# Kernel optimization log

Hardware: AMD Instinct MI355X
Metric: run time of the kernel (lower is better)

Reference implementation:

```python
import jax, jax.numpy as jnp
import numpy as np

H = 16          # num_heads
R = 4           # query compression ratio
WIN = 128       # sliding window size
NEG = -1e9      # finite mask value (safe softmax grads)


def setup_inputs() -> dict:
    key = jax.random.key(0)
    k0, k1, k2, k3, k4 = jax.random.split(key, 5)
    B, S, D = 4, 4096, 2048
    inputs = jax.random.normal(k0, (B, S, D), jnp.float32)
    attention_mask = jnp.ones((B, S), jnp.int32)
    s = 0.02
    Wq = jax.random.normal(k1, (D, D), jnp.float32) * s
    Wk = jax.random.normal(k2, (D, D), jnp.float32) * s
    Wv = jax.random.normal(k3, (D, D), jnp.float32) * s
    Wo = jax.random.normal(k4, (D, D), jnp.float32) * s
    return {"inputs": inputs, "attention_mask": attention_mask,
            "Wq": Wq, "Wk": Wk, "Wv": Wv, "Wo": Wo}


def _forward(inputs, attention_mask, Wq, Wk, Wv, Wo):
    B, S, D = inputs.shape
    dh = D // H
    scale = 1.0 / np.sqrt(dh).astype(np.float32)
    Cs = (S + R - 1) // R            # compressed query length (S % R == 0 here)
    win = min(WIN, S)
    ws = max(0, S - win)             # window start

    # Q projection -> [B,H,S,dh] -> compress groups of R by mean -> [B,H,Cs,dh]
    q = jnp.einsum('bsd,od->bso', inputs, Wq)
    q = q.reshape(B, S, H, dh).transpose(0, 2, 1, 3)
    qc = q.reshape(B, H, Cs, R, dh).mean(axis=3)

    # K/V only over the recent window
    wx = inputs[:, ws:ws + win, :]
    k = jnp.einsum('bsd,od->bso', wx, Wk).reshape(B, win, H, dh).transpose(0, 2, 1, 3)
    v = jnp.einsum('bsd,od->bso', wx, Wv).reshape(B, win, H, dh).transpose(0, 2, 1, 3)

    scores = jnp.einsum('bhqd,bhkd->bhqk', qc, k) * scale

    # causal mask: each compressed query sits at position (i+1)*R-1
    qpos = (jnp.arange(Cs) + 1) * R - 1                     # [Cs]
    wpos = ws + jnp.arange(win)
    causal = wpos[None, :] <= qpos[:, None]
    qbw = qpos < ws                                         # queries fully before window
    causal = causal.at[:, 0].set(causal[:, 0] | qbw)
    pad_ok = (attention_mask[:, ws:ws + win] != 0)
    full = causal[None, None, :, :] & pad_ok[:, None, None, :]

    scores = jnp.where(full, scores, NEG)
    weights = jax.nn.softmax(scores, axis=-1)
    out = jnp.einsum('bhqk,bhkd->bhqd', weights, v)         # [B,H,Cs,dh]
    out = out.transpose(0, 2, 1, 3).reshape(B, Cs, D)
    out = jnp.einsum('bsd,od->bso', out, Wo)

    if Cs != S:  # linear interpolation back to seq_len (align_corners=False)
        out = jax.image.resize(out, (B, S, D), method='linear')
    return out


def reference(inputs, attention_mask, Wq, Wk, Wv, Wo):
    return _forward(inputs, attention_mask, Wq, Wk, Wv, Wo)
```

## Files before the change

kernel.cpp:

```cpp
#include <hip/hip_runtime.h>
#include <hip/hip_bf16.h>


typedef __attribute__((ext_vector_type(8))) short short8;
typedef __attribute__((ext_vector_type(4))) short s16x4;
typedef __attribute__((ext_vector_type(4))) float f32x4;

#define LDP 72

#define QP_STRIDE  (128 * 2048)
#define KV_STRIDE  (512 * 2048)
#define YO_STRIDE  (132 * 2048)

__device__ __forceinline__ unsigned short f2bf(float f){
  unsigned int x = __float_as_uint(f);
  return (unsigned short)((x + 0x7fffu + ((x >> 16) & 1u)) >> 16);
}
__device__ __forceinline__ unsigned int pk2(float lo, float hi){
  return ((unsigned int)f2bf(hi) << 16) | (unsigned int)f2bf(lo);
}
__device__ __forceinline__ s16x4 cvt4(float4 v){
  union { __hip_bfloat162 h[2]; s16x4 s; } r;
  float2 a; a.x = v.x; a.y = v.y;
  float2 b; b.x = v.z; b.y = v.w;
  r.h[0] = __float22bfloat162_rn(a);
  r.h[1] = __float22bfloat162_rn(b);
  return r.s;
}
__device__ __forceinline__ short8 cvt8(float4 x, float4 y){
  union { s16x4 h[2]; short8 s; } r;
  r.h[0] = cvt4(x); r.h[1] = cvt4(y);
  return r.s;
}

__global__ __launch_bounds__(256) void prep_kernel(
    const float* __restrict__ inp,
    unsigned short* __restrict__ Awx, unsigned short* __restrict__ Aq)
{
  const int idx = blockIdx.x * 256 + threadIdx.x;
  if (blockIdx.y == 0){
    const int b = idx >> 15, rem = idx & 32767;
    const int j = rem >> 8, d8 = (rem & 255) * 8;
    const float* p = inp + ((size_t)b * 4096 + 3968 + j) * 2048 + d8;
    *(short8*)&Awx[((size_t)b * 128 + j) * 2048 + d8] =
        cvt8(*(const float4*)p, *(const float4*)(p + 4));
  } else {
    if (idx >= 32768) return;
    const int b = idx >> 13, rem = idx & 8191;
    const int c = rem >> 8, d8 = (rem & 255) * 8;
    const float* p = inp + ((size_t)b * 4096 + 3968 + 4 * c) * 2048 + d8;
    float4 x0 = *(const float4*)(p);
    float4 x1 = *(const float4*)(p + 2048);
    float4 x2 = *(const float4*)(p + 4096);
    float4 x3 = *(const float4*)(p + 6144);
    float4 y0 = *(const float4*)(p + 4);
    float4 y1 = *(const float4*)(p + 2052);
    float4 y2 = *(const float4*)(p + 4100);
    float4 y3 = *(const float4*)(p + 6148);
    float4 xm, ym;
    xm.x = 0.25f * (x0.x + x1.x + x2.x + x3.x);
    xm.y = 0.25f * (x0.y + x1.y + x2.y + x3.y);
    xm.z = 0.25f * (x0.z + x1.z + x2.z + x3.z);
    xm.w = 0.25f * (x0.w + x1.w + x2.w + x3.w);
    ym.x = 0.25f * (y0.x + y1.x + y2.x + y3.x);
    ym.y = 0.25f * (y0.y + y1.y + y2.y + y3.y);
    ym.z = 0.25f * (y0.z + y1.z + y2.z + y3.z);
    ym.w = 0.25f * (y0.w + y1.w + y2.w + y3.w);
    *(short8*)&Aq[((size_t)b * 32 + c) * 2048 + d8] = cvt8(xm, ym);
  }
}

__device__ __forceinline__ void gemm_body(
    const unsigned short* __restrict__ A, const float* __restrict__ W,
    float* __restrict__ Cp,
    int M, int row0, int n0, int kbase, int nsteps,
    unsigned short* As, unsigned short* Bs)
{
  const int tid  = threadIdx.x;
  const int lane = tid & 63;
  const int wid  = tid >> 6;
  const int wr = wid >> 1, wc = wid & 1;

  const int arow = tid >> 3;
  const int acol = (tid & 7) * 8;
  const int brow = tid >> 4;
  const int bcol = (tid & 15) * 4;

  f32x4 acc[4][2] = {};
  short8 ra[4];
  float4 rb[4];

  #pragma unroll
  for (int c = 0; c < 4; ++c){
    int gr = row0 + c * 32 + arow; if (gr > M - 1) gr = M - 1;
    ra[c] = *(const short8*)&A[(size_t)gr * 2048 + kbase + acol];
    rb[c] = *(const float4*)&W[(size_t)(n0 + c * 16 + brow) * 2048 + kbase + bcol];
  }
  #pragma unroll
  for (int c = 0; c < 4; ++c){
    *(short8*)&As[(c * 32 + arow) * LDP + acol] = ra[c];
    *(s16x4*)&Bs[(c * 16 + brow) * LDP + bcol] = cvt4(rb[c]);
  }
  __syncthreads();

  for (int t = 0; t < nsteps; ++t){
    const bool pf = (t + 1) < nsteps;
    if (pf){
      const int k0 = kbase + (t + 1) * 64;
      #pragma unroll
      for (int c = 0; c < 4; ++c){
        int gr = row0 + c * 32 + arow; if (gr > M - 1) gr = M - 1;
        ra[c] = *(const short8*)&A[(size_t)gr * 2048 + k0 + acol];
        rb[c] = *(const float4*)&W[(size_t)(n0 + c * 16 + brow) * 2048 + k0 + bcol];
      }
    }
    #pragma unroll
    for (int ks = 0; ks < 2; ++ks){
      short8 av[4], bv[2];
      #pragma unroll
      for (int f = 0; f < 4; ++f)
        av[f] = *(const short8*)&As[(wr * 64 + f * 16 + (lane & 15)) * LDP + ks * 32 + (lane >> 4) * 8];
      #pragma unroll
      for (int n = 0; n < 2; ++n)
        bv[n] = *(const short8*)&Bs[(wc * 32 + n * 16 + (lane & 15)) * LDP + ks * 32 + (lane >> 4) * 8];
      #pragma unroll
      for (int f = 0; f < 4; ++f)
        #pragma unroll
        for (int n = 0; n < 2; ++n)
          acc[f][n] = __builtin_amdgcn_mfma_f32_16x16x32_bf16(av[f], bv[n], acc[f][n], 0, 0, 0);
    }
    __syncthreads();
    if (pf){
      #pragma unroll
      for (int c = 0; c < 4; ++c){
        *(short8*)&As[(c * 32 + arow) * LDP + acol] = ra[c];
        *(s16x4*)&Bs[(c * 16 + brow) * LDP + bcol] = cvt4(rb[c]);
      }
      __syncthreads();
    }
  }

  #pragma unroll
  for (int f = 0; f < 4; ++f){
    #pragma unroll
    for (int n = 0; n < 2; ++n){
      const int col = n0 + wc * 32 + n * 16 + (lane & 15);
      #pragma unroll
      for (int r = 0; r < 4; ++r){
        const int row = row0 + wr * 64 + f * 16 + (lane >> 4) * 4 + r;
        if (row < M)
          Cp[(size_t)row * 2048 + col] = acc[f][n][r];
      }
    }
  }
}

__global__ __launch_bounds__(256, 4) void qkv_kernel(
    const unsigned short* __restrict__ Aq, const unsigned short* __restrict__ Awx,
    const float* __restrict__ Wq, const float* __restrict__ Wk, const float* __restrict__ Wv,
    float* __restrict__ Qp, float* __restrict__ Kp, float* __restrict__ Vp)
{
  __shared__ __align__(16) unsigned short As[128 * LDP];
  __shared__ __align__(16) unsigned short Bs[64 * LDP];
  const int nt = blockIdx.x, gy = blockIdx.y, ksp = blockIdx.z;
  if (gy == 0){
    if (ksp >= 2) return;
    gemm_body(Aq, Wq, Qp + (size_t)ksp * QP_STRIDE,
              128, 0, nt * 64, ksp * 1024, 16, As, Bs);
  } else if (gy < 5){
    gemm_body(Awx, Wk, Kp + (size_t)ksp * KV_STRIDE,
              512, (gy - 1) * 128, nt * 64, ksp * 512, 8, As, Bs);
  } else {
    gemm_body(Awx, Wv, Vp + (size_t)ksp * KV_STRIDE,
              512, (gy - 5) * 128, nt * 64, ksp * 512, 8, As, Bs);
  }
}

__global__ __launch_bounds__(256, 4) void o_kernel(
    const unsigned short* __restrict__ Ao, const float* __restrict__ Wo,
    float* __restrict__ Yop)
{
  __shared__ __align__(16) unsigned short As[128 * LDP];
  __shared__ __align__(16) unsigned short Bs[64 * LDP];
  gemm_body(Ao, Wo, Yop + (size_t)blockIdx.z * YO_STRIDE,
            132, blockIdx.y * 128, blockIdx.x * 64, blockIdx.z * 512, 8, As, Bs);
}

__global__ __launch_bounds__(256) void attn_kernel(
    const float* __restrict__ Qp, const float* __restrict__ Kp,
    const float* __restrict__ Vp, const int* __restrict__ amask,
    unsigned short* __restrict__ Ao)
{
  const int b = blockIdx.x >> 4;
  const int h = blockIdx.x & 15;
  __shared__ float Qs[32][129];
  __shared__ unsigned int Ks[128][65];
  __shared__ unsigned int Vs[128][65];
  __shared__ float Wt[32][132];
  __shared__ float msk[128];
  const int tid = threadIdx.x;

  for (int i = tid; i < 32 * 128; i += 256){
    int cq = i >> 7, d = i & 127;
    size_t off = (size_t)(b * 32 + cq) * 2048 + h * 128 + d;
    Qs[cq][d] = Qp[off] + Qp[off + QP_STRIDE];
  }
  for (int i = tid; i < 128 * 64; i += 256){
    int j = i >> 6, du = i & 63;
    size_t off = (size_t)(b * 128 + j) * 2048 + h * 128 + du * 2;
    float2 k0 = *(const float2*)(Kp + off);
    float2 k1 = *(const float2*)(Kp + off + KV_STRIDE);
    float2 k2 = *(const float2*)(Kp + off + 2 * KV_STRIDE);
    float2 k3 = *(const float2*)(Kp + off + 3 * KV_STRIDE);
    float2 v0 = *(const float2*)(Vp + off);
    float2 v1 = *(const float2*)(Vp + off + KV_STRIDE);
    float2 v2 = *(const float2*)(Vp + off + 2 * KV_STRIDE);
    float2 v3 = *(const float2*)(Vp + off + 3 * KV_STRIDE);
    Ks[j][du] = pk2(k0.x + k1.x + k2.x + k3.x, k0.y + k1.y + k2.y + k3.y);
    Vs[j][du] = pk2(v0.x + v1.x + v2.x + v3.x, v0.y + v1.y + v2.y + v3.y);
  }
  if (tid < 128){
    msk[tid] = (amask[b * 4096 + 3968 + tid] != 0) ? 1.f : 0.f;
    size_t off = (size_t)(b * 128) * 2048 + h * 128 + tid;
    Ao[(size_t)(b * 33) * 2048 + h * 128 + tid] =
        f2bf(Vp[off] + Vp[off + KV_STRIDE] + Vp[off + 2 * KV_STRIDE] + Vp[off + 3 * KV_STRIDE]);
  }
  __syncthreads();

  const int cq = tid >> 3, jg = tid & 7;
  const int jmax = 4 * cq + 3;
  const float scale = 0.088388347648318447f;

  float s[16];
  {
    float sacc[16];
    #pragma unroll
    for (int jj = 0; jj < 16; ++jj) sacc[jj] = 0.f;
    for (int du = 0; du < 64; ++du){
      float q0 = Qs[cq][2 * du], q1 = Qs[cq][2 * du + 1];
      #pragma unroll
      for (int jj = 0; jj < 16; ++jj){
        unsigned int u = Ks[jg * 16 + jj][du];
        sacc[jj] += q0 * __uint_as_float(u << 16) + q1 * __uint_as_float(u & 0xffff0000u);
      }
    }
    #pragma unroll
    for (int jj = 0; jj < 16; ++jj){
      int j = jg * 16 + jj;
      bool ok = (j <= jmax) && (msk[j] > 0.5f);
      s[jj] = ok ? sacc[jj] * scale : -1e9f;
    }
  }
  float m = s[0];
  #pragma unroll
  for (int jj = 1; jj < 16; ++jj) m = fmaxf(m, s[jj]);
  #pragma unroll
  for (int off = 1; off < 8; off <<= 1) m = fmaxf(m, __shfl_xor(m, off, 8));
  float sum = 0.f;
  #pragma unroll
  for (int jj = 0; jj < 16; ++jj){ s[jj] = expf(s[jj] - m); sum += s[jj]; }
  #pragma unroll
  for (int off = 1; off < 8; off <<= 1) sum += __shfl_xor(sum, off, 8);
  const float inv = 1.f / sum;
  #pragma unroll
  for (int jj = 0; jj < 16; ++jj) Wt[cq][jg * 16 + jj] = s[jj] * inv;
  __syncthreads();

  const int dg = tid & 7;
  float o[16];
  #pragma unroll
  for (int e = 0; e < 16; ++e) o[e] = 0.f;
  for (int j = 0; j < 128; ++j){
    float w = Wt[cq][j];
    #pragma unroll
    for (int du = 0; du < 8; ++du){
      unsigned int u = Vs[j][dg * 8 + du];
      o[2 * du]     += w * __uint_as_float(u << 16);
      o[2 * du + 1] += w * __uint_as_float(u & 0xffff0000u);
    }
  }
  unsigned short* dst = Ao + (size_t)(b * 33 + 1 + cq) * 2048 + h * 128 + dg * 16;
  #pragma unroll
  for (int e = 0; e < 16; ++e) dst[e] = f2bf(o[e]);
}

__global__ __launch_bounds__(256) void resize_kernel(
    const float* __restrict__ Yop, float* __restrict__ out)
{
  const int rowid = blockIdx.x;
  const int b = rowid >> 12;
  const int i = rowid & 4095;
  float c  = i * 0.25f - 0.375f;
  float fl = floorf(c);
  int   j0 = (int)fl;
  float f  = c - fl;
  int   j1 = j0 + 1;
  j0 = max(0, min(j0, 1023));
  j1 = max(0, min(j1, 1023));
  const int ri0 = b * 33 + (j0 <= 991 ? 0 : j0 - 991);
  const int ri1 = b * 33 + (j1 <= 991 ? 0 : j1 - 991);
  const float* r0 = Yop + (size_t)ri0 * 2048;
  const float* r1 = Yop + (size_t)ri1 * 2048;
  float* op = out + (size_t)rowid * 2048;
  const int t = threadIdx.x;
  const bool same = (ri0 == ri1);
  #pragma unroll
  for (int q = 0; q < 2; ++q){
    int d = q * 1024 + t * 4;
    float4 a0 = *(const float4*)(r0 + d);
    float4 a1 = *(const float4*)(r0 + d + YO_STRIDE);
    float4 a2 = *(const float4*)(r0 + d + 2 * YO_STRIDE);
    float4 a3 = *(const float4*)(r0 + d + 3 * YO_STRIDE);
    float4 a;
    a.x = a0.x + a1.x + a2.x + a3.x;
    a.y = a0.y + a1.y + a2.y + a3.y;
    a.z = a0.z + a1.z + a2.z + a3.z;
    a.w = a0.w + a1.w + a2.w + a3.w;
    float4 o = a;
    if (!same){
      float4 b0 = *(const float4*)(r1 + d);
      float4 b1 = *(const float4*)(r1 + d + YO_STRIDE);
      float4 b2 = *(const float4*)(r1 + d + 2 * YO_STRIDE);
      float4 b3 = *(const float4*)(r1 + d + 3 * YO_STRIDE);
      float4 bb;
      bb.x = b0.x + b1.x + b2.x + b3.x;
      bb.y = b0.y + b1.y + b2.y + b3.y;
      bb.z = b0.z + b1.z + b2.z + b3.z;
      bb.w = b0.w + b1.w + b2.w + b3.w;
      o.x = a.x + f * (bb.x - a.x);
      o.y = a.y + f * (bb.y - a.y);
      o.z = a.z + f * (bb.z - a.z);
      o.w = a.w + f * (bb.w - a.w);
    }
    *(float4*)(op + d) = o;
  }
}

extern "C" void kernel_launch(void* const* d_in, const int* in_sizes, int n_in,
                              void* d_out, int out_size, void* d_ws, size_t ws_size,
                              hipStream_t stream)
{
  const float* inp   = (const float*)d_in[0];
  const int*   amask = (const int*)d_in[1];
  const float* Wq = (const float*)d_in[2];
  const float* Wk = (const float*)d_in[3];
  const float* Wv = (const float*)d_in[4];
  const float* Wo = (const float*)d_in[5];
  float* out = (float*)d_out;

  char* ws = (char*)d_ws;
  unsigned short* Aq  = (unsigned short*)(ws);
  unsigned short* Awx = (unsigned short*)(ws + 524288);
  float*          Qp  = (float*)(ws + 2621440);
  float*          Kp  = (float*)(ws + 4718592);
  float*          Vp  = (float*)(ws + 21495808);
  float*          Yop = (float*)(ws + 38273024);
  unsigned short* Ao  = (unsigned short*)(ws + 42598400);

  prep_kernel<<<dim3(512, 2), 256, 0, stream>>>(inp, Awx, Aq);
  qkv_kernel<<<dim3(32, 9, 4), 256, 0, stream>>>(Aq, Awx, Wq, Wk, Wv, Qp, Kp, Vp);
  attn_kernel<<<64, 256, 0, stream>>>(Qp, Kp, Vp, amask, Ao);
  o_kernel<<<dim3(32, 2, 4), 256, 0, stream>>>(Ao, Wo, Yop);
  resize_kernel<<<16384, 256, 0, stream>>>(Yop, out);
}
```

Baseline: 117.5 us.

## Pre-convert weights to bf16, drop split-K in QKV GEMM, emit bf16 Q/K/V

A new prep stage converts all four weight matrices to bf16 in workspace, so the GEMMs load bf16 weight tiles directly instead of converting fp32 in the inner loop. The QKV GEMM no longer uses split-K partials: each block runs the full K=2048 reduction and writes bf16 outputs. Attention therefore reads bf16 Q/K/V directly without summing partials. The trade-off is an extra full pass over the 64MB of fp32 weights every call, plus fewer QKV blocks (288 instead of 1152) with longer serial K loops, which lowers parallelism.

Result: slower. 119.9 us (+2.0%).

```diff
diff --git a/kernel.cpp b/kernel.cpp
--- a/kernel.cpp
+++ b/kernel.cpp
@@ -7,17 +7,14 @@
 typedef __attribute__((ext_vector_type(4))) float f32x4;
 
 #define LDP 72
-
-#define QP_STRIDE  (128 * 2048)
-#define KV_STRIDE  (512 * 2048)
 #define YO_STRIDE  (132 * 2048)
 
 __device__ __forceinline__ unsigned short f2bf(float f){
   unsigned int x = __float_as_uint(f);
   return (unsigned short)((x + 0x7fffu + ((x >> 16) & 1u)) >> 16);
 }
-__device__ __forceinline__ unsigned int pk2(float lo, float hi){
-  return ((unsigned int)f2bf(hi) << 16) | (unsigned int)f2bf(lo);
+__device__ __forceinline__ float bf2f(unsigned short u){
+  return __uint_as_float(((unsigned int)u) << 16);
 }
 __device__ __forceinline__ s16x4 cvt4(float4 v){
   union { __hip_bfloat162 h[2]; s16x4 s; } r;
@@ -35,19 +32,33 @@
 
 __global__ __launch_bounds__(256) void prep_kernel(
     const float* __restrict__ inp,
+    const float* __restrict__ Wq, const float* __restrict__ Wk,
+    const float* __restrict__ Wv, const float* __restrict__ Wo,
+    unsigned short* __restrict__ Wb,
     unsigned short* __restrict__ Awx, unsigned short* __restrict__ Aq)
 {
-  const int idx = blockIdx.x * 256 + threadIdx.x;
-  if (blockIdx.y == 0){
-    const int b = idx >> 15, rem = idx & 32767;
-    const int j = rem >> 8, d8 = (rem & 255) * 8;
+  const int bx = blockIdx.x;
+  if (bx < 8192){
+    const int idx = bx * 256 + threadIdx.x;
+    const int w = idx >> 19;
+    const int sub = idx & 524287;
+    const float* src = (w == 0) ? Wq : (w == 1) ? Wk : (w == 2) ? Wv : Wo;
+    const float* p = src + (size_t)sub * 8;
+    *(short8*)&Wb[(size_t)w * 4194304 + (size_t)sub * 8] =
+        cvt8(*(const float4*)p, *(const float4*)(p + 4));
+  } else if (bx < 8704){
+    const int idx = (bx - 8192) * 256 + threadIdx.x;
+    const int b = idx >> 15;
+    const int j = (idx >> 8) & 127;
+    const int d8 = (idx & 255) * 8;
     const float* p = inp + ((size_t)b * 4096 + 3968 + j) * 2048 + d8;
     *(short8*)&Awx[((size_t)b * 128 + j) * 2048 + d8] =
         cvt8(*(const float4*)p, *(const float4*)(p + 4));
   } else {
-    if (idx >= 32768) return;
-    const int b = idx >> 13, rem = idx & 8191;
-    const int c = rem >> 8, d8 = (rem & 255) * 8;
+    const int idx = (bx - 8704) * 256 + threadIdx.x;
+    const int b = idx >> 13;
+    const int c = (idx >> 8) & 31;
+    const int d8 = (idx & 255) * 8;
     const float* p = inp + ((size_t)b * 4096 + 3968 + 4 * c) * 2048 + d8;
     float4 x0 = *(const float4*)(p);
     float4 x1 = *(const float4*)(p + 2048);
@@ -70,9 +81,10 @@
   }
 }
 
+template<bool OUT_BF16>
 __device__ __forceinline__ void gemm_body(
-    const unsigned short* __restrict__ A, const float* __restrict__ W,
-    float* __restrict__ Cp,
+    const unsigned short* __restrict__ A, const unsigned short* __restrict__ W,
+    unsigned short* __restrict__ Cb, float* __restrict__ Cf,
     int M, int row0, int n0, int kbase, int nsteps,
     unsigned short* As, unsigned short* Bs)
 {
@@ -81,26 +93,26 @@
   const int wid  = tid >> 6;
   const int wr = wid >> 1, wc = wid & 1;
 
-  const int arow = tid >> 3;
-  const int acol = (tid & 7) * 8;
-  const int brow = tid >> 4;
-  const int bcol = (tid & 15) * 4;
+  const int srow = tid >> 3;
+  const int scol = (tid & 7) * 8;
 
   f32x4 acc[4][2] = {};
-  short8 ra[4];
-  float4 rb[4];
+  short8 ra[4], rb[2];
 
   #pragma unroll
   for (int c = 0; c < 4; ++c){
-    int gr = row0 + c * 32 + arow; if (gr > M - 1) gr = M - 1;
-    ra[c] = *(const short8*)&A[(size_t)gr * 2048 + kbase + acol];
-    rb[c] = *(const float4*)&W[(size_t)(n0 + c * 16 + brow) * 2048 + kbase + bcol];
-  }
-  #pragma unroll
-  for (int c = 0; c < 4; ++c){
-    *(short8*)&As[(c * 32 + arow) * LDP + acol] = ra[c];
-    *(s16x4*)&Bs[(c * 16 + brow) * LDP + bcol] = cvt4(rb[c]);
-  }
+    int gr = row0 + c * 32 + srow; if (gr > M - 1) gr = M - 1;
+    ra[c] = *(const short8*)&A[(size_t)gr * 2048 + kbase + scol];
+  }
+  #pragma unroll
+  for (int c = 0; c < 2; ++c)
+    rb[c] = *(const short8*)&W[(size_t)(n0 + c * 32 + srow) * 2048 + kbase + scol];
+  #pragma unroll
+  for (int c = 0; c < 4; ++c)
+    *(short8*)&As[(c * 32 + srow) * LDP + scol] = ra[c];
+  #pragma unroll
+  for (int c = 0; c < 2; ++c)
+    *(short8*)&Bs[(c * 32 + srow) * LDP + scol] = rb[c];
   __syncthreads();
 
   for (int t = 0; t < nsteps; ++t){
@@ -109,10 +121,12 @@
       const int k0 = kbase + (t + 1) * 64;
       #pragma unroll
       for (int c = 0; c < 4; ++c){
-        int gr = row0 + c * 32 + arow; if (gr > M - 1) gr = M - 1;
-        ra[c] = *(const short8*)&A[(size_t)gr * 2048 + k0 + acol];
-        rb[c] = *(const float4*)&W[(size_t)(n0 + c * 16 + brow) * 2048 + k0 + bcol];
+        int gr = row0 + c * 32 + srow; if (gr > M - 1) gr = M - 1;
+        ra[c] = *(const short8*)&A[(size_t)gr * 2048 + k0 + scol];
       }
+      #pragma unroll
+      for (int c = 0; c < 2; ++c)
+        rb[c] = *(const short8*)&W[(size_t)(n0 + c * 32 + srow) * 2048 + k0 + scol];
     }
     #pragma unroll
     for (int ks = 0; ks < 2; ++ks){
@@ -132,10 +146,11 @@
     __syncthreads();
     if (pf){
       #pragma unroll
-      for (int c = 0; c < 4; ++c){
-        *(short8*)&As[(c * 32 + arow) * LDP + acol] = ra[c];
-        *(s16x4*)&Bs[(c * 16 + brow) * LDP + bcol] = cvt4(rb[c]);
-      }
+      for (int c = 0; c < 4; ++c)
+        *(short8*)&As[(c * 32 + srow) * LDP + scol] = ra[c];
+      #pragma unroll
+      for (int c = 0; c < 2; ++c)
+        *(short8*)&Bs[(c * 32 + srow) * LDP + scol] = rb[c];
       __syncthreads();
     }
   }
@@ -148,8 +163,10 @@
       #pragma unroll
       for (int r = 0; r < 4; ++r){
         const int row = row0 + wr * 64 + f * 16 + (lane >> 4) * 4 + r;
-        if (row < M)
-          Cp[(size_t)row * 2048 + col] = acc[f][n][r];
+        if (row < M){
+          if (OUT_BF16) Cb[(size_t)row * 2048 + col] = f2bf(acc[f][n][r]);
+          else          Cf[(size_t)row * 2048 + col] = acc[f][n][r];
+        }
       }
     }
   }
@@ -157,38 +174,34 @@
 
 __global__ __launch_bounds__(256, 4) void qkv_kernel(
     const unsigned short* __restrict__ Aq, const unsigned short* __restrict__ Awx,
-    const float* __restrict__ Wq, const float* __restrict__ Wk, const float* __restrict__ Wv,
-    float* __restrict__ Qp, float* __restrict__ Kp, float* __restrict__ Vp)
+    const unsigned short* __restrict__ Wb,
+    unsigned short* __restrict__ Qc, unsigned short* __restrict__ Kb,
+    unsigned short* __restrict__ Vb)
 {
   __shared__ __align__(16) unsigned short As[128 * LDP];
   __shared__ __align__(16) unsigned short Bs[64 * LDP];
-  const int nt = blockIdx.x, gy = blockIdx.y, ksp = blockIdx.z;
-  if (gy == 0){
-    if (ksp >= 2) return;
-    gemm_body(Aq, Wq, Qp + (size_t)ksp * QP_STRIDE,
-              128, 0, nt * 64, ksp * 1024, 16, As, Bs);
-  } else if (gy < 5){
-    gemm_body(Awx, Wk, Kp + (size_t)ksp * KV_STRIDE,
-              512, (gy - 1) * 128, nt * 64, ksp * 512, 8, As, Bs);
-  } else {
-    gemm_body(Awx, Wv, Vp + (size_t)ksp * KV_STRIDE,
-              512, (gy - 5) * 128, nt * 64, ksp * 512, 8, As, Bs);
-  }
+  const int nt = blockIdx.x, gy = blockIdx.y;
+  if (gy == 0)
+    gemm_body<true>(Aq,  Wb,            Qc, nullptr, 128, 0,              nt * 64, 0, 32, As, Bs);
+  else if (gy < 5)
+    gemm_body<true>(Awx, Wb + 4194304,  Kb, nullptr, 512, (gy - 1) * 128, nt * 64, 0, 32, As, Bs);
+  else
+    gemm_body<true>(Awx, Wb + 8388608,  Vb, nullptr, 512, (gy - 5) * 128, nt * 64, 0, 32, As, Bs);
 }
 
 __global__ __launch_bounds__(256, 4) void o_kernel(
-    const unsigned short* __restrict__ Ao, const float* __restrict__ Wo,
+    const unsigned short* __restrict__ Ao, const unsigned short* __restrict__ Wb,
     float* __restrict__ Yop)
 {
   __shared__ __align__(16) unsigned short As[128 * LDP];
   __shared__ __align__(16) unsigned short Bs[64 * LDP];
-  gemm_body(Ao, Wo, Yop + (size_t)blockIdx.z * YO_STRIDE,
-            132, blockIdx.y * 128, blockIdx.x * 64, blockIdx.z * 512, 8, As, Bs);
+  gemm_body<false>(Ao, Wb + 12582912, nullptr, Yop + (size_t)blockIdx.z * YO_STRIDE,
+                   132, blockIdx.y * 128, blockIdx.x * 64, blockIdx.z * 512, 8, As, Bs);
 }
 
 __global__ __launch_bounds__(256) void attn_kernel(
-    const float* __restrict__ Qp, const float* __restrict__ Kp,
-    const float* __restrict__ Vp, const int* __restrict__ amask,
+    const unsigned short* __restrict__ Qc, const unsigned short* __restrict__ Kb,
+    const unsigned short* __restrict__ Vb, const int* __restrict__ amask,
     unsigned short* __restrict__ Ao)
 {
   const int b = blockIdx.x >> 4;
@@ -202,28 +215,18 @@
 
   for (int i = tid; i < 32 * 128; i += 256){
     int cq = i >> 7, d = i & 127;
-    size_t off = (size_t)(b * 32 + cq) * 2048 + h * 128 + d;
-    Qs[cq][d] = Qp[off] + Qp[off + QP_STRIDE];
+    Qs[cq][d] = bf2f(Qc[(size_t)(b * 32 + cq) * 2048 + h * 128 + d]);
   }
   for (int i = tid; i < 128 * 64; i += 256){
     int j = i >> 6, du = i & 63;
-    size_t off = (size_t)(b * 128 + j) * 2048 + h * 128 + du * 2;
-    float2 k0 = *(const float2*)(Kp + off);
-    float2 k1 = *(const float2*)(Kp + off + KV_STRIDE);
-    float2 k2 = *(const float2*)(Kp + off + 2 * KV_STRIDE);
-    float2 k3 = *(const float2*)(Kp + off + 3 * KV_STRIDE);
-    float2 v0 = *(const float2*)(Vp + off);
-    float2 v1 = *(const float2*)(Vp + off + KV_STRIDE);
-    float2 v2 = *(const float2*)(Vp + off + 2 * KV_STRIDE);
-    float2 v3 = *(const float2*)(Vp + off + 3 * KV_STRIDE);
-    Ks[j][du] = pk2(k0.x + k1.x + k2.x + k3.x, k0.y + k1.y + k2.y + k3.y);
-    Vs[j][du] = pk2(v0.x + v1.x + v2.x + v3.x, v0.y + v1.y + v2.y + v3.y);
+    const unsigned int* kp = (const unsigned int*)(Kb + (size_t)(b * 128 + j) * 2048 + h * 128);
+    const unsigned int* vp = (const unsigned int*)(Vb + (size_t)(b * 128 + j) * 2048 + h * 128);
+    Ks[j][du] = kp[du];
+    Vs[j][du] = vp[du];
   }
   if (tid < 128){
     msk[tid] = (amask[b * 4096 + 3968 + tid] != 0) ? 1.f : 0.f;
-    size_t off = (size_t)(b * 128) * 2048 + h * 128 + tid;
-    Ao[(size_t)(b * 33) * 2048 + h * 128 + tid] =
-        f2bf(Vp[off] + Vp[off + KV_STRIDE] + Vp[off + 2 * KV_STRIDE] + Vp[off + 3 * KV_STRIDE]);
+    Ao[(size_t)(b * 33) * 2048 + h * 128 + tid] = Vb[(size_t)(b * 128) * 2048 + h * 128 + tid];
   }
   __syncthreads();
 
@@ -349,17 +352,18 @@
   float* out = (float*)d_out;
 
   char* ws = (char*)d_ws;
-  unsigned short* Aq  = (unsigned short*)(ws);
-  unsigned short* Awx = (unsigned short*)(ws + 524288);
-  float*          Qp  = (float*)(ws + 2621440);
-  float*          Kp  = (float*)(ws + 4718592);
-  float*          Vp  = (float*)(ws + 21495808);
-  float*          Yop = (float*)(ws + 38273024);
-  unsigned short* Ao  = (unsigned short*)(ws + 42598400);
-
-  prep_kernel<<<dim3(512, 2), 256, 0, stream>>>(inp, Awx, Aq);
-  qkv_kernel<<<dim3(32, 9, 4), 256, 0, stream>>>(Aq, Awx, Wq, Wk, Wv, Qp, Kp, Vp);
-  attn_kernel<<<64, 256, 0, stream>>>(Qp, Kp, Vp, amask, Ao);
-  o_kernel<<<dim3(32, 2, 4), 256, 0, stream>>>(Ao, Wo, Yop);
+  unsigned short* Wb  = (unsigned short*)(ws);
+  unsigned short* Aq  = (unsigned short*)(ws + 33554432);
+  unsigned short* Awx = (unsigned short*)(ws + 34078720);
+  unsigned short* Qc  = (unsigned short*)(ws + 36175872);
+  unsigned short* Kb  = (unsigned short*)(ws + 36700160);
+  unsigned short* Vb  = (unsigned short*)(ws + 38797312);
+  unsigned short* Ao  = (unsigned short*)(ws + 40894464);
+  float*          Yop = (float*)(ws + 41435136);
+
+  prep_kernel<<<8832, 256, 0, stream>>>(inp, Wq, Wk, Wv, Wo, Wb, Awx, Aq);
+  qkv_kernel<<<dim3(32, 9), 256, 0, stream>>>(Aq, Awx, Wb, Qc, Kb, Vb);
+  attn_kernel<<<64, 256, 0, stream>>>(Qc, Kb, Vb, amask, Ao);
+  o_kernel<<<dim3(32, 2, 4), 256, 0, stream>>>(Ao, Wb, Yop);
   resize_kernel<<<16384, 256, 0, stream>>>(Yop, out);
 }
```
